# Optimization experiments

Measured on AMD Instinct MI355X. Metric: run time of the kernel, lower is better.

The kernel has to match this reference:

```python
import jax, jax.numpy as jnp
import numpy as np

B, C, D = 32, 8192, 256
TOPK = 512


def find_confounders(w, sample_w, k):
    # squared euclidean distance [B, C] = |s|^2 - 2 s.w^T + |w|^2
    dis = (sample_w ** 2).sum(axis=1, keepdims=True) - 2.0 * sample_w @ w.T + (w ** 2).sum(axis=1)[None, :]
    _, idx = jax.lax.top_k(-dis, k)  # k smallest distances
    return idx


def setup_inputs() -> dict:
    key = jax.random.key(0)
    k1, k2, k3, k4, k5 = jax.random.split(key, 5)
    weight = jax.random.normal(k1, (C, D), dtype=jnp.float32)
    mu = jax.random.normal(k2, (B, D), dtype=jnp.float32)
    # keep variance bounded away from 0 for numerical sanity
    var = jax.random.uniform(k3, (B, D), dtype=jnp.float32) * 0.9 + 0.1
    all_class_density = jax.random.uniform(k4, (B, C, D), dtype=jnp.float32)
    labels = jax.random.randint(k5, (B,), 0, C, dtype=jnp.int64)
    nontrivial = jnp.ones((B, C, D), dtype=bool)
    return {"weight": weight, "mu": mu, "var": var,
            "all_class_density": all_class_density,
            "labels": labels, "nontrivial": nontrivial}


def reference(weight, mu, var, all_class_density, labels, nontrivial):
    sample_weight = weight[labels]                                  # [B, D]
    diff = jax.lax.stop_gradient(sample_weight - mu)                # detached in torch
    density = jnp.exp(-diff ** 2 / (2.0 * var))                     # [B, D]
    total_density = jnp.clip(all_class_density.sum(axis=1), 1e-8)   # [B, D]

    # method == 1 branch: mask out the per-(b,d) argmin class from nontrivial
    argmin_idx = jnp.argmin(all_class_density, axis=1)              # [B, D]
    kill = jnp.arange(C)[None, :, None] == argmin_idx[:, None, :]   # [B, C, D]
    nt = nontrivial & ~kill
    minv = (all_class_density + (~nt) * 1000.0).min(axis=1, keepdims=True)  # [B,1,D]
    maxv = (all_class_density - nt * 1000.0).max(axis=1, keepdims=True)     # [B,1,D]
    overly = (nt & (minv - maxv >= 0.2 * total_density[:, None, :])).astype(jnp.float32)

    confid = density[:, None, :] / total_density[:, None, :] * (1.0 - overly)  # [B, C, D]

    # penalize: renormalize by density over top-512 nearest confounder classes
    topkidx = find_confounders(weight, sample_weight, TOPK)         # [B, K]
    topk_w = weight[topkidx]                                        # [B, K, D]
    acd_det = jnp.exp(-jax.lax.stop_gradient(topk_w - mu[:, None, :]) ** 2 / (2.0 * var[:, None, :]))
    total_det = jnp.clip(acd_det.sum(axis=1), 1e-8)                 # [B, D]
    confid = confid - density[:, None, :] / total_det[:, None, :] * overly

    return confid.mean(axis=-1).mean()
```

## Files before the change

### kernel.cpp

```cpp
#include <hip/hip_runtime.h>
#include <cfloat>
#include <cstddef>

#define B_ 32
#define C_ 8192
#define D_ 256
#define K_ 512
#define NCH 32
#define CPB (C_ / NCH)

typedef float f4n __attribute__((ext_vector_type(4)));

__global__ __launch_bounds__(256) void k1_colreduce(const float* __restrict__ acd,
                                                    float* __restrict__ psum,
                                                    float* __restrict__ pm1,
                                                    float* __restrict__ pm2) {
    const int t = threadIdx.x;
    const int b = blockIdx.x / NCH, ch = blockIdx.x % NCH;
    const int d4 = t & 63;
    const int coff = t >> 6;

    const f4n* src = (const f4n*)(acd + ((size_t)b * C_ + (size_t)ch * CPB) * D_);

    f4n s  = (f4n){0.f, 0.f, 0.f, 0.f};
    f4n m1 = (f4n){FLT_MAX, FLT_MAX, FLT_MAX, FLT_MAX};
    f4n m2 = m1;

#define UPD3(f) { s.f += x.f; float mx = fmaxf(m1.f, x.f); m2.f = fminf(m2.f, mx); m1.f = fminf(m1.f, x.f); }
#pragma unroll 4
    for (int r = coff; r < CPB; r += 4) {
        f4n x = __builtin_nontemporal_load(&src[(size_t)r * 64 + d4]);
        UPD3(x) UPD3(y) UPD3(z) UPD3(w)
    }
#undef UPD3

    __shared__ f4n ls[256];
    __shared__ f4n l1[256];
    __shared__ f4n l2[256];
    ls[t] = s; l1[t] = m1; l2[t] = m2;
    __syncthreads();

    if (t < 64) {
        f4n S = ls[t], M1 = l1[t], M2 = l2[t];
#define CMB(f) { S.f += s2.f; float mx = fmaxf(M1.f, a1.f); M2.f = fminf(fminf(M2.f, a2.f), mx); M1.f = fminf(M1.f, a1.f); }
#pragma unroll
        for (int j = 64; j < 256; j += 64) {
            f4n s2 = ls[t + j], a1 = l1[t + j], a2 = l2[t + j];
            CMB(x) CMB(y) CMB(z) CMB(w)
        }
#undef CMB
        size_t o = ((size_t)b * NCH + ch) * 64 + t;
        ((f4n*)psum)[o] = S;
        ((f4n*)pm1)[o] = M1;
        ((f4n*)pm2)[o] = M2;
    }
}

__device__ __forceinline__ unsigned fmapk(float f) {
    unsigned u = __float_as_uint(f);
    return (u & 0x80000000u) ? ~u : (u | 0x80000000u);
}

__global__ __launch_bounds__(256) void k2_fused(const float* __restrict__ psum,
                                                const float* __restrict__ pm1,
                                                const float* __restrict__ pm2,
                                                const float* __restrict__ weight,
                                                const float* __restrict__ mu,
                                                const float* __restrict__ var,
                                                const int* __restrict__ labels,
                                                double* __restrict__ partial) {
    const int b = blockIdx.x, t = threadIdx.x;

    float sum = 0.f, m1 = FLT_MAX, m2 = FLT_MAX;
    for (int ch = 0; ch < NCH; ch++) {
        size_t o = ((size_t)b * NCH + ch) * D_ + t;
        float cs = psum[o], c1 = pm1[o], c2 = pm2[o];
        sum += cs;
        m2 = fminf(fminf(m2, c2), fmaxf(m1, c1));
        m1 = fminf(m1, c1);
    }
    const int lab = labels[b];
    const float sw = weight[(size_t)lab * D_ + t];
    const float muv = mu[b * D_ + t];
    const float v = var[b * D_ + t];
    const float diff = sw - muv;
    const float dens = expf(-(diff * diff) / (2.0f * v));
    const float tot = fmaxf(sum, 1e-8f);
    const float o_ = (m2 - m1 >= 0.2f * tot) ? 1.0f : 0.0f;

    double contrib = (double)dens / (double)tot *
                     ((double)C_ - (double)(C_ - 1) * (double)o_);

    __shared__ unsigned anyo;
    if (t == 0) anyo = 0u;
    __syncthreads();
    if (o_ != 0.0f) atomicOr(&anyo, 1u);
    __syncthreads();

    if (anyo != 0u) {
        __shared__ unsigned kl[C_];
        __shared__ float s_s[D_];
        __shared__ unsigned hist[256];
        __shared__ unsigned scan[256];
        __shared__ int sel[K_];
        __shared__ unsigned sh_pref, sh_want, sh_nsel;

        s_s[t] = sw;
        if (t == 0) { sh_pref = 0u; sh_want = K_; sh_nsel = 0u; }
        __syncthreads();

        for (int c = t; c < C_; c += 256) {
            const f4n* wr = (const f4n*)(weight + (size_t)c * D_);
            const f4n* sr = (const f4n*)s_s;
            float dot = 0.f, nsq = 0.f;
#pragma unroll 8
            for (int d4 = 0; d4 < D_ / 4; d4++) {
                f4n w = wr[d4], sv = sr[d4];
                dot += w.x * sv.x + w.y * sv.y + w.z * sv.z + w.w * sv.w;
                nsq += w.x * w.x + w.y * w.y + w.z * w.z + w.w * w.w;
            }
            kl[c] = fmapk(nsq - 2.0f * dot);
        }
        __syncthreads();

        for (int pass = 0; pass < 4; pass++) {
            const int shift = 24 - 8 * pass;
            hist[t] = 0u;
            __syncthreads();
            const unsigned pref = sh_pref;
            const unsigned pmask = (pass == 0) ? 0u : (0xFFFFFFFFu << (shift + 8));
            for (int c = t; c < C_; c += 256) {
                unsigned u = kl[c];
                if ((u & pmask) == (pref & pmask)) atomicAdd(&hist[(u >> shift) & 255u], 1u);
            }
            __syncthreads();
            unsigned h = hist[t];
            scan[t] = h;
            __syncthreads();
            for (int off = 1; off < 256; off <<= 1) {
                unsigned x = (t >= off) ? scan[t - off] : 0u;
                __syncthreads();
                scan[t] += x;
                __syncthreads();
            }
            const unsigned want = sh_want;
            const unsigned incl = scan[t], excl = incl - h;
            if (incl >= want && excl < want) {
                sh_pref = pref | ((unsigned)t << shift);
                sh_want = want - excl;
            }
            __syncthreads();
        }

        const unsigned Kk = sh_pref, quota = sh_want;
        for (int c = t; c < C_; c += 256) {
            unsigned u = kl[c];
            bool take = (u < Kk);
            if (!take && u == Kk) {
                unsigned r = 0;
                for (int j = 0; j < c; j++)
                    if (kl[j] == Kk) r++;
                take = (r < quota);
            }
            if (take) {
                unsigned s2 = atomicAdd(&sh_nsel, 1u);
                sel[s2] = c;
            }
        }
        __syncthreads();

        const float nh = -0.5f / v;
        float acc = 0.f;
        for (int k = 0; k < K_; k++) {
            float w = weight[(size_t)sel[k] * D_ + t];
            float df = w - muv;
            acc += expf(df * df * nh);
        }
        double td = fmax((double)acc, 1e-8);
        contrib -= (double)dens / td * (double)(C_ - 1) * (double)o_;
    }

    __shared__ double red[256];
    red[t] = contrib;
    __syncthreads();
    for (int s2 = 128; s2 > 0; s2 >>= 1) {
        if (t < s2) red[t] += red[t + s2];
        __syncthreads();
    }
    if (t == 0) partial[b] = red[0];
}

__global__ __launch_bounds__(64) void k3_final(const double* __restrict__ partial,
                                               float* __restrict__ out) {
    const int t = threadIdx.x;
    double v = (t < B_) ? partial[t] : 0.0;
#pragma unroll
    for (int off = 32; off > 0; off >>= 1) v += __shfl_down(v, off);
    if (t == 0) out[0] = (float)(v / ((double)B_ * (double)C_ * (double)D_));
}

extern "C" void kernel_launch(void* const* d_in, const int* in_sizes, int n_in,
                              void* d_out, int out_size, void* d_ws, size_t ws_size,
                              hipStream_t stream) {
    const float* weight = (const float*)d_in[0];
    const float* mu     = (const float*)d_in[1];
    const float* var    = (const float*)d_in[2];
    const float* acd    = (const float*)d_in[3];
    const int*   labels = (const int*)d_in[4];
    float* out = (float*)d_out;

    char* ws = (char*)d_ws;
    const size_t np = (size_t)B_ * NCH * D_;
    float* psum = (float*)ws;
    float* pm1  = psum + np;
    float* pm2  = pm1 + np;
    double* partial = (double*)(pm2 + np);

    k1_colreduce<<<B_ * NCH, 256, 0, stream>>>(acd, psum, pm1, pm2);
    k2_fused<<<B_, 256, 0, stream>>>(psum, pm1, pm2, weight, mu, var, labels, partial);
    k3_final<<<1, 64, 0, stream>>>(partial, out);
}
```

Baseline: 448.2 us.

## Fuse column reduction, top-k penalty and final sum via last-block atomic counters

Merges the three kernels into one grid, with a small init kernel that zeroes atomic counters. The last chunk block finishing for each batch row runs the per-row selection and penalty work, and the last row block does the final reduction. Shared memory is overlaid across phases to fit in one block. This removes launch gaps and lets the per-row tail overlap with other rows' streaming, at the cost of larger shared memory per block, which can lower occupancy during the bandwidth-bound reduction phase.

New measurement: 584.3 us. 1.3x slower.

```diff
diff --git a/kernel.cpp b/kernel.cpp
--- a/kernel.cpp
+++ b/kernel.cpp
@@ -11,73 +11,94 @@
 
 typedef float f4n __attribute__((ext_vector_type(4)));
 
-__global__ __launch_bounds__(256) void k1_colreduce(const float* __restrict__ acd,
-                                                    float* __restrict__ psum,
-                                                    float* __restrict__ pm1,
-                                                    float* __restrict__ pm2) {
-    const int t = threadIdx.x;
-    const int b = blockIdx.x / NCH, ch = blockIdx.x % NCH;
-    const int d4 = t & 63;
-    const int coff = t >> 6;
-
-    const f4n* src = (const f4n*)(acd + ((size_t)b * C_ + (size_t)ch * CPB) * D_);
-
-    f4n s  = (f4n){0.f, 0.f, 0.f, 0.f};
-    f4n m1 = (f4n){FLT_MAX, FLT_MAX, FLT_MAX, FLT_MAX};
-    f4n m2 = m1;
-
-#define UPD3(f) { s.f += x.f; float mx = fmaxf(m1.f, x.f); m2.f = fminf(m2.f, mx); m1.f = fminf(m1.f, x.f); }
-#pragma unroll 4
-    for (int r = coff; r < CPB; r += 4) {
-        f4n x = __builtin_nontemporal_load(&src[(size_t)r * 64 + d4]);
-        UPD3(x) UPD3(y) UPD3(z) UPD3(w)
-    }
-#undef UPD3
-
-    __shared__ f4n ls[256];
-    __shared__ f4n l1[256];
-    __shared__ f4n l2[256];
-    ls[t] = s; l1[t] = m1; l2[t] = m2;
-    __syncthreads();
-
-    if (t < 64) {
-        f4n S = ls[t], M1 = l1[t], M2 = l2[t];
-#define CMB(f) { S.f += s2.f; float mx = fmaxf(M1.f, a1.f); M2.f = fminf(fminf(M2.f, a2.f), mx); M1.f = fminf(M1.f, a1.f); }
-#pragma unroll
-        for (int j = 64; j < 256; j += 64) {
-            f4n s2 = ls[t + j], a1 = l1[t + j], a2 = l2[t + j];
-            CMB(x) CMB(y) CMB(z) CMB(w)
-        }
-#undef CMB
-        size_t o = ((size_t)b * NCH + ch) * 64 + t;
-        ((f4n*)psum)[o] = S;
-        ((f4n*)pm1)[o] = M1;
-        ((f4n*)pm2)[o] = M2;
-    }
-}
-
 __device__ __forceinline__ unsigned fmapk(float f) {
     unsigned u = __float_as_uint(f);
     return (u & 0x80000000u) ? ~u : (u | 0x80000000u);
 }
 
-__global__ __launch_bounds__(256) void k2_fused(const float* __restrict__ psum,
-                                                const float* __restrict__ pm1,
-                                                const float* __restrict__ pm2,
-                                                const float* __restrict__ weight,
-                                                const float* __restrict__ mu,
-                                                const float* __restrict__ var,
-                                                const int* __restrict__ labels,
-                                                double* __restrict__ partial) {
-    const int b = blockIdx.x, t = threadIdx.x;
+__global__ __launch_bounds__(64) void k0_init(unsigned* __restrict__ cnt) {
+    if (threadIdx.x <= B_) cnt[threadIdx.x] = 0u;
+}
+
+__global__ __launch_bounds__(256) void k_fused(const float* __restrict__ acd,
+                                               const float* __restrict__ weight,
+                                               const float* __restrict__ mu,
+                                               const float* __restrict__ var,
+                                               const int* __restrict__ labels,
+                                               float* __restrict__ psum,
+                                               float* __restrict__ pm1,
+                                               float* __restrict__ pm2,
+                                               double* __restrict__ partial,
+                                               unsigned* __restrict__ cnt,
+                                               float* __restrict__ out) {
+    const int t = threadIdx.x;
+    const int b = blockIdx.x / NCH, ch = blockIdx.x % NCH;
+
+    __shared__ __align__(16) char smem[37888];
+    f4n* ls = (f4n*)smem;
+    f4n* l1 = (f4n*)(smem + 4096);
+    f4n* l2 = (f4n*)(smem + 8192);
+    unsigned* kl   = (unsigned*)smem;
+    float*    s_s  = (float*)(smem + 32768);
+    unsigned* hist = (unsigned*)(smem + 33792);
+    unsigned* scan = (unsigned*)(smem + 34816);
+    int*      sel  = (int*)(smem + 35840);
+    double*   red  = (double*)smem;
+    __shared__ unsigned s_fin, s_anyo, s_last, sh_pref, sh_want, sh_nsel;
+
+    {
+        const int d4 = t & 63;
+        const int coff = t >> 6;
+        const f4n* src = (const f4n*)(acd + ((size_t)b * C_ + (size_t)ch * CPB) * D_);
+
+        f4n s  = (f4n){0.f, 0.f, 0.f, 0.f};
+        f4n m1 = (f4n){FLT_MAX, FLT_MAX, FLT_MAX, FLT_MAX};
+        f4n m2 = m1;
+
+#define UPD3(f) { s.f += x.f; float mx = fmaxf(m1.f, x.f); m2.f = fminf(m2.f, mx); m1.f = fminf(m1.f, x.f); }
+#pragma unroll 4
+        for (int r = coff; r < CPB; r += 4) {
+            f4n x = __builtin_nontemporal_load(&src[(size_t)r * 64 + d4]);
+            UPD3(x) UPD3(y) UPD3(z) UPD3(w)
+        }
+#undef UPD3
+
+        ls[t] = s; l1[t] = m1; l2[t] = m2;
+        __syncthreads();
+
+        if (t < 64) {
+            f4n S = ls[t], M1 = l1[t], M2 = l2[t];
+#define CMB(f) { S.f += s2.f; float mx = fmaxf(M1.f, a1.f); M2.f = fminf(fminf(M2.f, a2.f), mx); M1.f = fminf(M1.f, a1.f); }
+#pragma unroll
+            for (int j = 64; j < 256; j += 64) {
+                f4n s2 = ls[t + j], a1 = l1[t + j], a2 = l2[t + j];
+                CMB(x) CMB(y) CMB(z) CMB(w)
+            }
+#undef CMB
+            size_t o = ((size_t)b * NCH + ch) * 64 + t;
+            ((f4n*)psum)[o] = S;
+            ((f4n*)pm1)[o] = M1;
+            ((f4n*)pm2)[o] = M2;
+        }
+    }
+
+    __threadfence();
+    __syncthreads();
+    if (t == 0) {
+        s_fin = (atomicAdd(&cnt[b], 1u) == NCH - 1) ? 1u : 0u;
+        s_last = 0u;
+    }
+    __syncthreads();
+    if (s_fin == 0u) return;
+    __threadfence();
 
     float sum = 0.f, m1 = FLT_MAX, m2 = FLT_MAX;
-    for (int ch = 0; ch < NCH; ch++) {
-        size_t o = ((size_t)b * NCH + ch) * D_ + t;
-        float cs = psum[o], c1 = pm1[o], c2 = pm2[o];
+    for (int c2 = 0; c2 < NCH; c2++) {
+        size_t o = ((size_t)b * NCH + c2) * D_ + t;
+        float cs = psum[o], c1v = pm1[o], c2v = pm2[o];
         sum += cs;
-        m2 = fminf(fminf(m2, c2), fmaxf(m1, c1));
-        m1 = fminf(m1, c1);
+        m2 = fminf(fminf(m2, c2v), fmaxf(m1, c1v));
+        m1 = fminf(m1, c1v);
     }
     const int lab = labels[b];
     const float sw = weight[(size_t)lab * D_ + t];
@@ -91,20 +112,12 @@
     double contrib = (double)dens / (double)tot *
                      ((double)C_ - (double)(C_ - 1) * (double)o_);
 
-    __shared__ unsigned anyo;
-    if (t == 0) anyo = 0u;
-    __syncthreads();
-    if (o_ != 0.0f) atomicOr(&anyo, 1u);
-    __syncthreads();
-
-    if (anyo != 0u) {
-        __shared__ unsigned kl[C_];
-        __shared__ float s_s[D_];
-        __shared__ unsigned hist[256];
-        __shared__ unsigned scan[256];
-        __shared__ int sel[K_];
-        __shared__ unsigned sh_pref, sh_want, sh_nsel;
-
+    if (t == 0) s_anyo = 0u;
+    __syncthreads();
+    if (o_ != 0.0f) atomicOr(&s_anyo, 1u);
+    __syncthreads();
+
+    if (s_anyo != 0u) {
         s_s[t] = sw;
         if (t == 0) { sh_pref = 0u; sh_want = K_; sh_nsel = 0u; }
         __syncthreads();
@@ -163,8 +176,8 @@
                 take = (r < quota);
             }
             if (take) {
-                unsigned s2 = atomicAdd(&sh_nsel, 1u);
-                sel[s2] = c;
+                unsigned s2i = atomicAdd(&sh_nsel, 1u);
+                if (s2i < (unsigned)K_) sel[s2i] = c;
             }
         }
         __syncthreads();
@@ -178,25 +191,28 @@
         }
         double td = fmax((double)acc, 1e-8);
         contrib -= (double)dens / td * (double)(C_ - 1) * (double)o_;
-    }
-
-    __shared__ double red[256];
+        __syncthreads();
+    }
+
     red[t] = contrib;
     __syncthreads();
     for (int s2 = 128; s2 > 0; s2 >>= 1) {
         if (t < s2) red[t] += red[t + s2];
         __syncthreads();
     }
-    if (t == 0) partial[b] = red[0];
-}
-
-__global__ __launch_bounds__(64) void k3_final(const double* __restrict__ partial,
-                                               float* __restrict__ out) {
-    const int t = threadIdx.x;
-    double v = (t < B_) ? partial[t] : 0.0;
+    if (t == 0) {
+        partial[b] = red[0];
+        __threadfence();
+        s_last = (atomicAdd(&cnt[B_], 1u) == B_ - 1) ? 1u : 0u;
+    }
+    __syncthreads();
+    if (s_last != 0u && t < 64) {
+        __threadfence();
+        double v2 = (t < B_) ? partial[t] : 0.0;
 #pragma unroll
-    for (int off = 32; off > 0; off >>= 1) v += __shfl_down(v, off);
-    if (t == 0) out[0] = (float)(v / ((double)B_ * (double)C_ * (double)D_));
+        for (int off = 32; off > 0; off >>= 1) v2 += __shfl_down(v2, off);
+        if (t == 0) out[0] = (float)(v2 / ((double)B_ * (double)C_ * (double)D_));
+    }
 }
 
 extern "C" void kernel_launch(void* const* d_in, const int* in_sizes, int n_in,
@@ -215,8 +231,9 @@
     float* pm1  = psum + np;
     float* pm2  = pm1 + np;
     double* partial = (double*)(pm2 + np);
-
-    k1_colreduce<<<B_ * NCH, 256, 0, stream>>>(acd, psum, pm1, pm2);
-    k2_fused<<<B_, 256, 0, stream>>>(psum, pm1, pm2, weight, mu, var, labels, partial);
-    k3_final<<<1, 64, 0, stream>>>(partial, out);
-}
+    unsigned* cnt = (unsigned*)(partial + B_);
+
+    k0_init<<<1, 64, 0, stream>>>(cnt);
+    k_fused<<<B_ * NCH, 256, 0, stream>>>(acd, weight, mu, var, labels,
+                                          psum, pm1, pm2, partial, cnt, out);
+}
```
